# Kernel tuning notes

Measured on AMD Instinct MI355X. Metric: run time of the kernel, lower is better.

Reference implementation:

```python
import jax, jax.numpy as jnp
import numpy as np
from jax import lax

B, N, M, D = 32, 256, 256, 512
NEG = -1e9  # matches deepblast's -1e10-style padding of V borders


def _nw_score(theta, A):
    """Soft (softmax-operator) Needleman-Wunsch terminal score V[N, M].

    theta, A: [N, M]. Recurrence (deepblast _forward_pass):
      V[i, j] = theta[i-1, j-1] + logsumexp(A[i-1, j-1] + V[i-1, j],
                                            V[i-1, j-1],
                                            A[i-1, j-1] + V[i, j-1])
    with V[0, 0] = 0 and borders -inf. Implemented as a row scan with an
    inner column scan (left dependency is sequential within a row).
    """
    n, m = theta.shape
    dt = theta.dtype

    def row_step(prev_row, xs):
        # prev_row: V[i-1, 0..M]  (length m+1)
        th_row, a_row = xs  # each [m]

        def col_step(v_left, c):
            v_diag, v_up, th, a = c
            v = th + jax.nn.logsumexp(jnp.stack([a + v_up, v_diag, a + v_left]))
            return v, v

        _, row = lax.scan(col_step, jnp.asarray(NEG, dt),
                          (prev_row[:-1], prev_row[1:], th_row, a_row))
        new_row = jnp.concatenate([jnp.full((1,), NEG, dt), row])
        return new_row, None

    init = jnp.concatenate([jnp.zeros((1,), dt), jnp.full((m,), NEG, dt)])
    last_row, _ = lax.scan(row_step, init, (theta, A))
    return last_row[-1]  # V[N, M]


def _nw_decode(theta, A):
    # deepblast's decode returns E = dV_t/dtheta (expected alignment matrix);
    # with the softmax operator this is exactly the gradient of the terminal
    # score, so autodiff reproduces the hand-written backward pass.
    return jax.grad(_nw_score, argnums=0)(theta, A)


def setup_inputs() -> dict:
    key = jax.random.key(0)
    k1, k2, k3, k4 = jax.random.split(key, 4)
    s = D ** -0.25  # so bid,bjd dot products are ~N(0, 1)
    zx = jax.random.normal(k1, (B, N, D), jnp.float32) * s
    zy = jax.random.normal(k2, (B, M, D), jnp.float32) * s
    gx = jax.random.normal(k3, (B, N, D), jnp.float32) * s
    gy = jax.random.normal(k4, (B, M, D), jnp.float32) * s
    return {"zx": zx, "zy": zy, "gx": gx, "gy": gy}


def reference(zx, zy, gx, gy):
    theta = jax.nn.softplus(jnp.einsum('bid,bjd->bij', zx, zy))  # [B,N,M]
    A = jax.nn.log_sigmoid(jnp.einsum('bid,bjd->bij', gx, gy))   # [B,N,M]
    aln = jax.vmap(_nw_decode)(theta, A)                          # [B,N,M]
    return aln, theta, A
```

## Files before the change

kernel.cpp:

```cpp
#include <hip/hip_runtime.h>
#include <hip/hip_bf16.h>
#include <hip/hip_fp16.h>
#include <cstdint>
#include <cstddef>

#define BB 32
#define NN 256
#define MM 256
#define DD 512
#define NEGF (-1e9f)
#define LOG2E 1.4426950408889634f
#define SPLN 82176
#define QPLN 82176
#define EPLN 81920

typedef __fp16 h2 __attribute__((ext_vector_type(2)));
typedef float f32x4_t __attribute__((ext_vector_type(4)));
typedef unsigned int u32x4_t __attribute__((ext_vector_type(4)));
typedef short s16x8 __attribute__((ext_vector_type(8)));

__device__ __forceinline__ uint32_t pack_q(float a, float b) {
  h2 r = __builtin_amdgcn_cvt_pkrtz(a, b);
  return __builtin_bit_cast(uint32_t, r);
}
__device__ __forceinline__ float2 unpack_q(uint32_t u) {
  h2 r = __builtin_bit_cast(h2, u);
  return make_float2((float)r.x, (float)r.y);
}
__device__ __forceinline__ float softplus_f(float x) {
  return fmaxf(x, 0.f) + __logf(1.f + __expf(-fabsf(x)));
}
__device__ __forceinline__ float logsig_f(float x) {
  return fminf(x, 0.f) - __logf(1.f + __expf(-fabsf(x)));
}
__device__ __forceinline__ short f2bf(float f) {
  uint32_t u = __builtin_bit_cast(uint32_t, f);
  u += 0x7FFFu + ((u >> 16) & 1u);
  return (short)(u >> 16);
}

#define WAITV(N) do { \
  asm volatile("s_waitcnt vmcnt(" #N ")" ::: "memory"); \
  __builtin_amdgcn_sched_barrier(0); \
} while (0)

#define DRAIN() do { \
  asm volatile("s_waitcnt vmcnt(0) lgkmcnt(0)" ::: "memory"); \
  __builtin_amdgcn_sched_barrier(0); \
} while (0)

#define SBAR() __builtin_amdgcn_sched_barrier(0)

__global__ __launch_bounds__(256) void gemm_mfma(const float* __restrict__ ZX,
                                                 const float* __restrict__ ZY,
                                                 const float* __restrict__ GX,
                                                 const float* __restrict__ GY,
                                                 float* __restrict__ theta,
                                                 float* __restrict__ Amat,
                                                 float* __restrict__ thS,
                                                 float* __restrict__ aS) {
  const int z  = blockIdx.z;
  const int b  = z & 31;
  const int op = z >> 5;
  const int ty = blockIdx.y;
  const int tx = blockIdx.x;
  const float* Xb = (op ? GX : ZX) + (size_t)b * NN * DD;
  const float* Yb = (op ? GY : ZY) + (size_t)b * MM * DD;
  float* outb = (op ? Amat : theta) + (size_t)b * NN * MM;
  float* skb  = (op ? aS : thS) + (size_t)b * SPLN;

  __shared__ short xs[64][40];
  __shared__ short ys[64][40];

  const int tid = threadIdx.x;
  const int l   = tid & 63;
  const int w   = tid >> 6;
  const int r0  = (w >> 1) * 32;
  const int c0  = (w & 1) * 32;
  const int srow = tid >> 2;
  const int scg  = (tid & 3) * 8;

  f32x4_t acc[2][2];
  #pragma unroll
  for (int i = 0; i < 2; ++i)
    #pragma unroll
    for (int j = 0; j < 2; ++j) acc[i][j] = f32x4_t{0.f, 0.f, 0.f, 0.f};

  const int lr = l & 15;
  const int kof = (l >> 4) * 8;

  for (int ks = 0; ks < 16; ++ks) {
    const int k0 = ks * 32;
    const float4 xv0 = *(const float4*)(Xb + (size_t)(ty * 64 + srow) * DD + k0 + scg);
    const float4 xv1 = *(const float4*)(Xb + (size_t)(ty * 64 + srow) * DD + k0 + scg + 4);
    const float4 yv0 = *(const float4*)(Yb + (size_t)(tx * 64 + srow) * DD + k0 + scg);
    const float4 yv1 = *(const float4*)(Yb + (size_t)(tx * 64 + srow) * DD + k0 + scg + 4);
    __syncthreads();
    s16x8 xp, yp;
    xp[0] = f2bf(xv0.x); xp[1] = f2bf(xv0.y); xp[2] = f2bf(xv0.z); xp[3] = f2bf(xv0.w);
    xp[4] = f2bf(xv1.x); xp[5] = f2bf(xv1.y); xp[6] = f2bf(xv1.z); xp[7] = f2bf(xv1.w);
    yp[0] = f2bf(yv0.x); yp[1] = f2bf(yv0.y); yp[2] = f2bf(yv0.z); yp[3] = f2bf(yv0.w);
    yp[4] = f2bf(yv1.x); yp[5] = f2bf(yv1.y); yp[6] = f2bf(yv1.z); yp[7] = f2bf(yv1.w);
    *(s16x8*)&xs[srow][scg] = xp;
    *(s16x8*)&ys[srow][scg] = yp;
    __syncthreads();
    const s16x8 a0 = *(const s16x8*)&xs[r0 + lr][kof];
    const s16x8 a1 = *(const s16x8*)&xs[r0 + 16 + lr][kof];
    const s16x8 b0 = *(const s16x8*)&ys[c0 + lr][kof];
    const s16x8 b1 = *(const s16x8*)&ys[c0 + 16 + lr][kof];
    acc[0][0] = __builtin_amdgcn_mfma_f32_16x16x32_bf16(a0, b0, acc[0][0], 0, 0, 0);
    acc[0][1] = __builtin_amdgcn_mfma_f32_16x16x32_bf16(a0, b1, acc[0][1], 0, 0, 0);
    acc[1][0] = __builtin_amdgcn_mfma_f32_16x16x32_bf16(a1, b0, acc[1][0], 0, 0, 0);
    acc[1][1] = __builtin_amdgcn_mfma_f32_16x16x32_bf16(a1, b1, acc[1][1], 0, 0, 0);
  }

  #pragma unroll
  for (int i = 0; i < 2; ++i) {
    #pragma unroll
    for (int j = 0; j < 2; ++j) {
      #pragma unroll
      for (int r = 0; r < 4; ++r) {
        const int R = ty * 64 + r0 + i * 16 + (l >> 4) * 4 + r;
        const int C = tx * 64 + c0 + j * 16 + (l & 15);
        const float v = acc[i][j][r];
        const float act = (op == 0) ? softplus_f(v) : logsig_f(v);
        outb[(size_t)R * MM + C] = act;
        skb[(size_t)(C + 1 + (R >> 2)) * 256 + R] = act * LOG2E;
      }
    }
  }
}

__global__ __launch_bounds__(64, 1) void nw_wave(const float* __restrict__ thSA,
                                                 const float* __restrict__ aSA,
                                                 u32x4_t* __restrict__ qSA,
                                                 float* __restrict__ eSA) {
  const int b = blockIdx.x;
  const int t = threadIdx.x;
  const float* thS = thSA + (size_t)b * SPLN;
  const float* aS  = aSA  + (size_t)b * SPLN;
  u32x4_t* qS = qSA + (size_t)b * (QPLN / 4);
  float* eSb = eSA + (size_t)b * EPLN;

  __shared__ f32x4_t stg[24][64];

  float vp[4];
  #pragma unroll
  for (int k = 0; k < 4; ++k) vp[k] = NEGF;
  float vu_sh = NEGF, vd_sh = NEGF;

  auto fstage = [&](int rbase, int mlo) {
    #pragma unroll
    for (int q = 0; q < 4; ++q) {
      int m = mlo + q; m = m < 1 ? 1 : (m > 320 ? 320 : m);
      __builtin_amdgcn_global_load_lds((const void*)(thS + (size_t)m * 256 + 4 * t),
                                       (void*)&stg[rbase + q][0], 16, 0, 0);
      __builtin_amdgcn_global_load_lds((const void*)(aS + (size_t)m * 256 + 4 * t),
                                       (void*)&stg[rbase + 4 + q][0], 16, 0, 0);
    }
  };

  fstage(0, 1); fstage(8, 5); fstage(16, 9);
  u32x4_t* qpt = qS + 64 + t;
  for (int h = 0; h < 80; ++h) {
    const int m0 = 1 + 4 * h;
    const int R = (h % 3) * 8;
    if (h == 0)      WAITV(16);
    else if (h == 1) WAITV(20);
    else             WAITV(24);
    f32x4_t thc = stg[R][t], ac = stg[R + 4][t];
    f32x4_t thn, an;
    #pragma unroll
    for (int u = 0; u < 4; ++u) {
      if (u < 3) { thn = stg[R + u + 1][t]; an = stg[R + 4 + u + 1][t]; }
      SBAR();
      const int m = m0 + u;
      const int j = m - t;
      const bool actv = (j >= 1) && (j <= 256);
      float vu_in = vu_sh, vd_in = vd_sh;
      if (t == 0) { vu_in = NEGF; vd_in = (m == 1) ? 0.f : NEGF; }
      float x2v[4], m12[4];
      #pragma unroll
      for (int k = 0; k < 4; ++k) {
        x2v[k] = ac[k] + vp[k];
        const float vdk = (k == 0) ? vd_in : vp[k - 1];
        m12[k] = fmaxf(vdk, x2v[k]);
      }
      float vn[4];
      uint32_t pk[4];
      #pragma unroll
      for (int k = 0; k < 4; ++k) {
        const float vu  = (k == 0) ? vu_in : vn[k - 1];
        const float vdk = (k == 0) ? vd_in : vp[k - 1];
        const float x0 = ac[k] + vu;
        const float mx = fmaxf(x0, m12[k]);
        const float e0 = __builtin_amdgcn_exp2f(x0 - mx);
        const float e1 = __builtin_amdgcn_exp2f(vdk - mx);
        const float e2 = __builtin_amdgcn_exp2f(x2v[k] - mx);
        const float Z  = e0 + e1 + e2;
        const float rz = __builtin_amdgcn_rcpf(Z);
        const float v  = thc[k] + mx + __builtin_amdgcn_logf(Z);
        vn[k] = actv ? v : vp[k];
        pk[k] = pack_q(e0 * rz, e2 * rz);
      }
      qpt[0] = u32x4_t{pk[0], pk[1], pk[2], pk[3]};
      qpt += 64;
      const float nsh = __shfl_up(vn[3], 1);
      vd_sh = vu_sh; vu_sh = nsh;
      #pragma unroll
      for (int k = 0; k < 4; ++k) vp[k] = vn[k];
      if (u < 3) { thc = thn; ac = an; }
    }
    fstage(R, m0 + 12);
  }

  DRAIN();

  float ep[4] = {0.f, 0.f, 0.f, 0.f};
  float sh_e1 = 0.f, sh_e2 = 0.f;
  uint32_t sh_q1 = 0u, sh_q2 = 0u;
  u32x4_t qm1 = u32x4_t{0u, 0u, 0u, 0u};
  const u32x4_t QONE = u32x4_t{0x3C00u, 0x3C00u, 0x3C00u, 0x3C00u};

  auto bstage = [&](int rbase, int Phi) {
    #pragma unroll
    for (int u = 0; u < 4; ++u) {
      int P = Phi - u; P = P < 0 ? 0 : (P > 320 ? 320 : P);
      __builtin_amdgcn_global_load_lds((const void*)(qS + (size_t)P * 64 + t),
                                       (void*)&stg[rbase + u][0], 16, 0, 0);
    }
  };

  bstage(0, 319); bstage(4, 315); bstage(8, 311);
  float* eptr = eSb + 4 * t;
  for (int n = 0; n < 80; ++n) {
    const int R = (n % 3) * 4;
    if (n == 0)      WAITV(8);
    else if (n == 1) WAITV(12);
    else             WAITV(16);
    u32x4_t cur = __builtin_bit_cast(u32x4_t, stg[R][t]);
    u32x4_t nxt;
    #pragma unroll
    for (int u = 0; u < 4; ++u) {
      if (u < 3) nxt = __builtin_bit_cast(u32x4_t, stg[R + u + 1][t]);
      SBAR();
      const int mp = 4 * n + u;
      const int P  = 319 - mp;
      const int j  = P - t;
      const bool actv = (j >= 1) && (j <= 256);
      const bool jok  = (j <= 255);
      const u32x4_t qmm = jok ? qm1 : QONE;
      const uint32_t sq1 = (t == 63) ? 0u : sh_q1;
      const uint32_t sq2 = (t == 63 || !jok) ? 0x3C00u : sh_q2;
      float en[4];
      #pragma unroll
      for (int kk = 0; kk < 4; ++kk) {
        const int k = 3 - kk;
        const uint32_t uA = (k < 3) ? cur[k + 1] : sq1;
        const uint32_t uB = (k < 3) ? qmm[k + 1] : sq2;
        const uint32_t uC = qmm[k];
        const float2 fA = unpack_q(uA);
        const float2 fB = unpack_q(uB);
        const float2 fC = unpack_q(uC);
        const float q1u = fA.x;
        const float q2d = 1.f - fB.x - fB.y;
        const float q3l = fC.y;
        const float eu = (k < 3) ? en[k + 1] : sh_e1;
        const float ed = (k < 3) ? ep[k + 1] : sh_e2;
        const float el = ep[k];
        float E = q1u * eu + q2d * ed + q3l * el;
        if (n == 0 && u == 0 && k == 3) E = (t == 63) ? 1.f : E;
        en[k] = actv ? E : 0.f;
      }
      *(f32x4_t*)eptr = f32x4_t{en[0], en[1], en[2], en[3]};
      eptr += 256;
      const float ne = __shfl_down(en[0], 1);
      sh_e2 = sh_e1; sh_e1 = ne;
      const uint32_t nq = (uint32_t)__shfl_down((int)cur[0], 1);
      sh_q2 = sh_q1; sh_q1 = nq;
      ep[0] = en[0]; ep[1] = en[1]; ep[2] = en[2]; ep[3] = en[3];
      qm1 = cur;
      if (u < 3) cur = nxt;
    }
    bstage(R, 307 - 4 * n);
  }
}

__global__ __launch_bounds__(256) void untwist(const float* __restrict__ eS,
                                               float* __restrict__ aln) {
  const int b  = blockIdx.z;
  const int r0 = blockIdx.y * 64;
  const int c0 = blockIdx.x * 64;
  const int tid = threadIdx.x;
  const float* ep = eS + (size_t)b * EPLN;

  __shared__ float ld[80][65];

  const int lx = tid & 63;
  const int wy = tid >> 6;
  const int mbase = 240 - c0 - (r0 >> 2);
  #pragma unroll
  for (int k = 0; k < 20; ++k) {
    const int p = wy + 4 * k;
    ld[p][lx] = ep[(size_t)(mbase + p) * 256 + r0 + lx];
  }
  __syncthreads();
  #pragma unroll
  for (int k = 0; k < 16; ++k) {
    const int rr = wy + 4 * k;
    aln[(size_t)b * NN * MM + (size_t)(r0 + rr) * MM + c0 + lx] =
        ld[78 - lx - (rr >> 2)][rr];
  }
}

extern "C" void kernel_launch(void* const* d_in, const int* in_sizes, int n_in,
                              void* d_out, int out_size, void* d_ws, size_t ws_size,
                              hipStream_t stream) {
  const float* zx = (const float*)d_in[0];
  const float* zy = (const float*)d_in[1];
  const float* gx = (const float*)d_in[2];
  const float* gy = (const float*)d_in[3];

  float* out   = (float*)d_out;
  float* aln   = out;
  float* theta = out + (size_t)BB * NN * MM;
  float* Amat  = out + (size_t)2 * BB * NN * MM;

  float* ws  = (float*)d_ws;
  float* thS = ws;
  float* aS  = ws + (size_t)BB * SPLN;
  u32x4_t* qS = (u32x4_t*)(ws + (size_t)2 * BB * SPLN);
  float* eS = ws + (size_t)3 * BB * SPLN;

  gemm_mfma<<<dim3(4, 4, 64), 256, 0, stream>>>(zx, zy, gx, gy,
                                                theta, Amat, thS, aS);
  nw_wave<<<BB, 64, 0, stream>>>(thS, aS, qS, eS);
  untwist<<<dim3(4, 4, BB), 256, 0, stream>>>(eS, aln);
}
```

Before: 170.3 us.

## Write backward pass results directly to aln and drop untwist kernel; deepen forward staging

The backward wavefront now scatters each thread's four E values straight into the final aln matrix, using a dummy per-thread slot for inactive lanes. This removes the intermediate skewed E buffer and the separate untwist transpose kernel and its launch. The forward pass stages 8 anti-diagonals per batch instead of 4, doubling the LDS staging area, and the shuffle is moved ahead of the probability packing to overlap its latency. The direct stores are strided by row (non-coalesced), and the backward wait counts were changed to account for the new store traffic.

```diff
diff --git a/kernel.cpp b/kernel.cpp
--- a/kernel.cpp
+++ b/kernel.cpp
@@ -12,7 +12,6 @@
 #define LOG2E 1.4426950408889634f
 #define SPLN 82176
 #define QPLN 82176
-#define EPLN 81920
 
 typedef __fp16 h2 __attribute__((ext_vector_type(2)));
 typedef float f32x4_t __attribute__((ext_vector_type(4)));
@@ -134,45 +133,47 @@
 __global__ __launch_bounds__(64, 1) void nw_wave(const float* __restrict__ thSA,
                                                  const float* __restrict__ aSA,
                                                  u32x4_t* __restrict__ qSA,
-                                                 float* __restrict__ eSA) {
+                                                 float* __restrict__ aln,
+                                                 float* __restrict__ dmpA) {
   const int b = blockIdx.x;
   const int t = threadIdx.x;
   const float* thS = thSA + (size_t)b * SPLN;
   const float* aS  = aSA  + (size_t)b * SPLN;
   u32x4_t* qS = qSA + (size_t)b * (QPLN / 4);
-  float* eSb = eSA + (size_t)b * EPLN;
-
-  __shared__ f32x4_t stg[24][64];
+  float* ALN = aln + (size_t)b * NN * MM;
+  float* dmp = dmpA + (size_t)b * 64 + t;
+
+  __shared__ f32x4_t stg[48][64];
 
   float vp[4];
   #pragma unroll
   for (int k = 0; k < 4; ++k) vp[k] = NEGF;
   float vu_sh = NEGF, vd_sh = NEGF;
 
-  auto fstage = [&](int rbase, int mlo) {
-    #pragma unroll
-    for (int q = 0; q < 4; ++q) {
+  auto fstage8 = [&](int rbase, int mlo) {
+    #pragma unroll
+    for (int q = 0; q < 8; ++q) {
       int m = mlo + q; m = m < 1 ? 1 : (m > 320 ? 320 : m);
       __builtin_amdgcn_global_load_lds((const void*)(thS + (size_t)m * 256 + 4 * t),
                                        (void*)&stg[rbase + q][0], 16, 0, 0);
       __builtin_amdgcn_global_load_lds((const void*)(aS + (size_t)m * 256 + 4 * t),
-                                       (void*)&stg[rbase + 4 + q][0], 16, 0, 0);
+                                       (void*)&stg[rbase + 8 + q][0], 16, 0, 0);
     }
   };
 
-  fstage(0, 1); fstage(8, 5); fstage(16, 9);
+  fstage8(0, 1); fstage8(16, 9); fstage8(32, 17);
   u32x4_t* qpt = qS + 64 + t;
-  for (int h = 0; h < 80; ++h) {
-    const int m0 = 1 + 4 * h;
-    const int R = (h % 3) * 8;
-    if (h == 0)      WAITV(16);
-    else if (h == 1) WAITV(20);
-    else             WAITV(24);
-    f32x4_t thc = stg[R][t], ac = stg[R + 4][t];
+  for (int h = 0; h < 40; ++h) {
+    const int m0 = 1 + 8 * h;
+    const int R = (h % 3) * 16;
+    if (h == 0)      WAITV(32);
+    else if (h == 1) WAITV(40);
+    else             WAITV(48);
+    f32x4_t thc = stg[R][t], ac = stg[R + 8][t];
     f32x4_t thn, an;
     #pragma unroll
-    for (int u = 0; u < 4; ++u) {
-      if (u < 3) { thn = stg[R + u + 1][t]; an = stg[R + 4 + u + 1][t]; }
+    for (int u = 0; u < 8; ++u) {
+      if (u < 7) { thn = stg[R + u + 1][t]; an = stg[R + 8 + u + 1][t]; }
       SBAR();
       const int m = m0 + u;
       const int j = m - t;
@@ -186,8 +187,7 @@
         const float vdk = (k == 0) ? vd_in : vp[k - 1];
         m12[k] = fmaxf(vdk, x2v[k]);
       }
-      float vn[4];
-      uint32_t pk[4];
+      float vn[4], e0v[4], e2v[4], rzv[4];
       #pragma unroll
       for (int k = 0; k < 4; ++k) {
         const float vu  = (k == 0) ? vu_in : vn[k - 1];
@@ -198,20 +198,24 @@
         const float e1 = __builtin_amdgcn_exp2f(vdk - mx);
         const float e2 = __builtin_amdgcn_exp2f(x2v[k] - mx);
         const float Z  = e0 + e1 + e2;
-        const float rz = __builtin_amdgcn_rcpf(Z);
+        rzv[k] = __builtin_amdgcn_rcpf(Z);
         const float v  = thc[k] + mx + __builtin_amdgcn_logf(Z);
         vn[k] = actv ? v : vp[k];
-        pk[k] = pack_q(e0 * rz, e2 * rz);
+        e0v[k] = e0; e2v[k] = e2;
       }
+      const float nsh = __shfl_up(vn[3], 1);
+      uint32_t pk[4];
+      #pragma unroll
+      for (int k = 0; k < 4; ++k)
+        pk[k] = pack_q(e0v[k] * rzv[k], e2v[k] * rzv[k]);
       qpt[0] = u32x4_t{pk[0], pk[1], pk[2], pk[3]};
       qpt += 64;
-      const float nsh = __shfl_up(vn[3], 1);
       vd_sh = vu_sh; vu_sh = nsh;
       #pragma unroll
       for (int k = 0; k < 4; ++k) vp[k] = vn[k];
-      if (u < 3) { thc = thn; ac = an; }
-    }
-    fstage(R, m0 + 12);
+      if (u < 7) { thc = thn; ac = an; }
+    }
+    fstage8(R, m0 + 24);
   }
 
   DRAIN();
@@ -232,12 +236,11 @@
   };
 
   bstage(0, 319); bstage(4, 315); bstage(8, 311);
-  float* eptr = eSb + 4 * t;
   for (int n = 0; n < 80; ++n) {
     const int R = (n % 3) * 4;
     if (n == 0)      WAITV(8);
-    else if (n == 1) WAITV(12);
-    else             WAITV(16);
+    else if (n == 1) WAITV(24);
+    else             WAITV(40);
     u32x4_t cur = __builtin_bit_cast(u32x4_t, stg[R][t]);
     u32x4_t nxt;
     #pragma unroll
@@ -272,44 +275,18 @@
         if (n == 0 && u == 0 && k == 3) E = (t == 63) ? 1.f : E;
         en[k] = actv ? E : 0.f;
       }
-      *(f32x4_t*)eptr = f32x4_t{en[0], en[1], en[2], en[3]};
-      eptr += 256;
       const float ne = __shfl_down(en[0], 1);
+      const uint32_t nq = (uint32_t)__shfl_down((int)cur[0], 1);
+      float* bp = actv ? (ALN + (size_t)(4 * t) * MM + (j - 1)) : dmp;
+      const int st = actv ? MM : 0;
+      bp[0] = en[0]; bp[st] = en[1]; bp[2 * st] = en[2]; bp[3 * st] = en[3];
       sh_e2 = sh_e1; sh_e1 = ne;
-      const uint32_t nq = (uint32_t)__shfl_down((int)cur[0], 1);
       sh_q2 = sh_q1; sh_q1 = nq;
       ep[0] = en[0]; ep[1] = en[1]; ep[2] = en[2]; ep[3] = en[3];
       qm1 = cur;
       if (u < 3) cur = nxt;
     }
     bstage(R, 307 - 4 * n);
-  }
-}
-
-__global__ __launch_bounds__(256) void untwist(const float* __restrict__ eS,
-                                               float* __restrict__ aln) {
-  const int b  = blockIdx.z;
-  const int r0 = blockIdx.y * 64;
-  const int c0 = blockIdx.x * 64;
-  const int tid = threadIdx.x;
-  const float* ep = eS + (size_t)b * EPLN;
-
-  __shared__ float ld[80][65];
-
-  const int lx = tid & 63;
-  const int wy = tid >> 6;
-  const int mbase = 240 - c0 - (r0 >> 2);
-  #pragma unroll
-  for (int k = 0; k < 20; ++k) {
-    const int p = wy + 4 * k;
-    ld[p][lx] = ep[(size_t)(mbase + p) * 256 + r0 + lx];
-  }
-  __syncthreads();
-  #pragma unroll
-  for (int k = 0; k < 16; ++k) {
-    const int rr = wy + 4 * k;
-    aln[(size_t)b * NN * MM + (size_t)(r0 + rr) * MM + c0 + lx] =
-        ld[78 - lx - (rr >> 2)][rr];
   }
 }
 
@@ -330,10 +307,9 @@
   float* thS = ws;
   float* aS  = ws + (size_t)BB * SPLN;
   u32x4_t* qS = (u32x4_t*)(ws + (size_t)2 * BB * SPLN);
-  float* eS = ws + (size_t)3 * BB * SPLN;
+  float* dmp = ws + (size_t)3 * BB * SPLN;
 
   gemm_mfma<<<dim3(4, 4, 64), 256, 0, stream>>>(zx, zy, gx, gy,
                                                 theta, Amat, thS, aS);
-  nw_wave<<<BB, 64, 0, stream>>>(thS, aS, qS, eS);
-  untwist<<<dim3(4, 4, BB), 256, 0, stream>>>(eS, aln);
-}
+  nw_wave<<<BB, 64, 0, stream>>>(thS, aS, qS, aln, dmp);
+}
```

Measured after the change: 173.6 us. No clear change (+1.9%).

## Split NW wavefront across two waves with 2 rows per lane and interleaved skew layout

Applied to the files above, without the earlier changes.

The soft-NW forward and backward wavefronts now run on 128 threads (two waves) per batch instead of one, with each lane owning 2 rows instead of 4. This shortens the serial dependency chain per anti-diagonal step. The two waves exchange boundary values through shared memory with a workgroup barrier every step. Theta and A are interleaved into one skewed plane so a single async load fetches both, and q is stored per-step instead of staged. The cost is more diagonal steps (383 instead of 319), a barrier per step, and larger workspace and untwist footprints.

```diff
diff --git a/kernel.cpp b/kernel.cpp
--- a/kernel.cpp
+++ b/kernel.cpp
@@ -10,9 +10,9 @@
 #define DD 512
 #define NEGF (-1e9f)
 #define LOG2E 1.4426950408889634f
-#define SPLN 82176
-#define QPLN 82176
-#define EPLN 81920
+#define SKWN 196608
+#define QPN  98304
+#define EPN  98304
 
 typedef __fp16 h2 __attribute__((ext_vector_type(2)));
 typedef float f32x4_t __attribute__((ext_vector_type(4)));
@@ -49,7 +49,12 @@
   __builtin_amdgcn_sched_barrier(0); \
 } while (0)
 
-#define SBAR() __builtin_amdgcn_sched_barrier(0)
+#define STEPBAR() do { \
+  asm volatile("s_waitcnt lgkmcnt(0)" ::: "memory"); \
+  __builtin_amdgcn_sched_barrier(0); \
+  __builtin_amdgcn_s_barrier(); \
+  asm volatile("" ::: "memory"); \
+} while (0)
 
 __global__ __launch_bounds__(256) void gemm_mfma(const float* __restrict__ ZX,
                                                  const float* __restrict__ ZY,
@@ -57,8 +62,7 @@
                                                  const float* __restrict__ GY,
                                                  float* __restrict__ theta,
                                                  float* __restrict__ Amat,
-                                                 float* __restrict__ thS,
-                                                 float* __restrict__ aS) {
+                                                 float* __restrict__ skw) {
   const int z  = blockIdx.z;
   const int b  = z & 31;
   const int op = z >> 5;
@@ -67,7 +71,7 @@
   const float* Xb = (op ? GX : ZX) + (size_t)b * NN * DD;
   const float* Yb = (op ? GY : ZY) + (size_t)b * MM * DD;
   float* outb = (op ? Amat : theta) + (size_t)b * NN * MM;
-  float* skb  = (op ? aS : thS) + (size_t)b * SPLN;
+  float* skb  = skw + (size_t)b * SKWN;
 
   __shared__ short xs[64][40];
   __shared__ short ys[64][40];
@@ -125,164 +129,176 @@
         const float v = acc[i][j][r];
         const float act = (op == 0) ? softplus_f(v) : logsig_f(v);
         outb[(size_t)R * MM + C] = act;
-        skb[(size_t)(C + 1 + (R >> 2)) * 256 + R] = act * LOG2E;
+        const int m = (C + 1) + (R >> 1);
+        skb[(size_t)m * 512 + ((R >> 1) << 2) + (op ? 2 : 0) + (R & 1)] =
+            act * LOG2E;
       }
     }
   }
 }
 
-__global__ __launch_bounds__(64, 1) void nw_wave(const float* __restrict__ thSA,
-                                                 const float* __restrict__ aSA,
-                                                 u32x4_t* __restrict__ qSA,
-                                                 float* __restrict__ eSA) {
+__global__ __launch_bounds__(128, 1) void nw_wave(const float* __restrict__ skwA,
+                                                  uint32_t* __restrict__ qSA,
+                                                  float* __restrict__ eSA) {
   const int b = blockIdx.x;
   const int t = threadIdx.x;
-  const float* thS = thSA + (size_t)b * SPLN;
-  const float* aS  = aSA  + (size_t)b * SPLN;
-  u32x4_t* qS = qSA + (size_t)b * (QPLN / 4);
-  float* eSb = eSA + (size_t)b * EPLN;
-
-  __shared__ f32x4_t stg[24][64];
-
-  float vp[4];
-  #pragma unroll
-  for (int k = 0; k < 4; ++k) vp[k] = NEGF;
+  const int w64 = (t >> 6) << 6;
+  const float* skw = skwA + (size_t)b * SKWN;
+  uint32_t* qS = qSA + (size_t)b * QPN;
+  float* eSb = eSA + (size_t)b * EPN;
+
+  __shared__ f32x4_t stg[12][128];
+  __shared__ uint32_t qstg[12][256];
+  __shared__ float xv[3];
+  __shared__ float xe[3];
+  __shared__ uint32_t xq[3];
+
+  if (t < 3) { xv[t] = NEGF; xe[t] = 0.f; xq[t] = 0u; }
+  __syncthreads();
+
+  float vp[2] = {NEGF, NEGF};
   float vu_sh = NEGF, vd_sh = NEGF;
 
   auto fstage = [&](int rbase, int mlo) {
     #pragma unroll
     for (int q = 0; q < 4; ++q) {
-      int m = mlo + q; m = m < 1 ? 1 : (m > 320 ? 320 : m);
-      __builtin_amdgcn_global_load_lds((const void*)(thS + (size_t)m * 256 + 4 * t),
-                                       (void*)&stg[rbase + q][0], 16, 0, 0);
-      __builtin_amdgcn_global_load_lds((const void*)(aS + (size_t)m * 256 + 4 * t),
-                                       (void*)&stg[rbase + 4 + q][0], 16, 0, 0);
+      int m = mlo + q; m = m < 1 ? 1 : (m > 383 ? 383 : m);
+      __builtin_amdgcn_global_load_lds((const void*)(skw + (size_t)m * 512 + 4 * t),
+                                       (void*)&stg[rbase + q][w64], 16, 0, 0);
     }
   };
 
-  fstage(0, 1); fstage(8, 5); fstage(16, 9);
-  u32x4_t* qpt = qS + 64 + t;
-  for (int h = 0; h < 80; ++h) {
+  fstage(0, 1); fstage(4, 5); fstage(8, 9);
+  for (int h = 0; h < 96; ++h) {
     const int m0 = 1 + 4 * h;
-    const int R = (h % 3) * 8;
-    if (h == 0)      WAITV(16);
-    else if (h == 1) WAITV(20);
-    else             WAITV(24);
-    f32x4_t thc = stg[R][t], ac = stg[R + 4][t];
-    f32x4_t thn, an;
+    const int R = (h % 3) * 4;
+    if (h == 0)      WAITV(8);
+    else if (h == 1) WAITV(12);
+    else             WAITV(16);
+    f32x4_t c4 = stg[R][t];
+    f32x4_t n4;
     #pragma unroll
     for (int u = 0; u < 4; ++u) {
-      if (u < 3) { thn = stg[R + u + 1][t]; an = stg[R + 4 + u + 1][t]; }
-      SBAR();
+      if (u < 3) n4 = stg[R + u + 1][t];
       const int m = m0 + u;
+      const float xvr1 = xv[(m + 2) % 3];
+      const float xvr2 = xv[(m + 1) % 3];
+      __builtin_amdgcn_sched_barrier(0);
       const int j = m - t;
       const bool actv = (j >= 1) && (j <= 256);
-      float vu_in = vu_sh, vd_in = vd_sh;
+      float vu_in = (t == 64) ? xvr1 : vu_sh;
+      float vd_in = (t == 64) ? xvr2 : vd_sh;
       if (t == 0) { vu_in = NEGF; vd_in = (m == 1) ? 0.f : NEGF; }
-      float x2v[4], m12[4];
+      float vn[2];
+      uint32_t pk[2];
       #pragma unroll
-      for (int k = 0; k < 4; ++k) {
-        x2v[k] = ac[k] + vp[k];
-        const float vdk = (k == 0) ? vd_in : vp[k - 1];
-        m12[k] = fmaxf(vdk, x2v[k]);
-      }
-      float vn[4];
-      uint32_t pk[4];
-      #pragma unroll
-      for (int k = 0; k < 4; ++k) {
-        const float vu  = (k == 0) ? vu_in : vn[k - 1];
-        const float vdk = (k == 0) ? vd_in : vp[k - 1];
-        const float x0 = ac[k] + vu;
-        const float mx = fmaxf(x0, m12[k]);
+      for (int k = 0; k < 2; ++k) {
+        const float vu  = (k == 0) ? vu_in : vn[0];
+        const float vdk = (k == 0) ? vd_in : vp[0];
+        const float vl  = vp[k];
+        const float a  = c4[2 + k];
+        const float th = c4[k];
+        const float x0 = a + vu;
+        const float x2 = a + vl;
+        const float mx = fmaxf(fmaxf(x0, vdk), x2);
         const float e0 = __builtin_amdgcn_exp2f(x0 - mx);
         const float e1 = __builtin_amdgcn_exp2f(vdk - mx);
-        const float e2 = __builtin_amdgcn_exp2f(x2v[k] - mx);
+        const float e2 = __builtin_amdgcn_exp2f(x2 - mx);
         const float Z  = e0 + e1 + e2;
         const float rz = __builtin_amdgcn_rcpf(Z);
-        const float v  = thc[k] + mx + __builtin_amdgcn_logf(Z);
+        const float v  = th + mx + __builtin_amdgcn_logf(Z);
         vn[k] = actv ? v : vp[k];
         pk[k] = pack_q(e0 * rz, e2 * rz);
       }
-      qpt[0] = u32x4_t{pk[0], pk[1], pk[2], pk[3]};
-      qpt += 64;
-      const float nsh = __shfl_up(vn[3], 1);
+      const float nsh = __shfl_up(vn[1], 1);
+      const int ms = (m <= 383) ? m : 0;
+      *(uint2*)(qS + (size_t)ms * 256 + 2 * t) = make_uint2(pk[0], pk[1]);
+      if (t == 63) xv[m % 3] = vn[1];
       vd_sh = vu_sh; vu_sh = nsh;
-      #pragma unroll
-      for (int k = 0; k < 4; ++k) vp[k] = vn[k];
-      if (u < 3) { thc = thn; ac = an; }
+      vp[0] = vn[0]; vp[1] = vn[1];
+      if (u < 3) c4 = n4;
+      STEPBAR();
     }
     fstage(R, m0 + 12);
   }
 
   DRAIN();
-
-  float ep[4] = {0.f, 0.f, 0.f, 0.f};
+  __builtin_amdgcn_s_barrier();
+
+  float ep[2] = {0.f, 0.f};
   float sh_e1 = 0.f, sh_e2 = 0.f;
   uint32_t sh_q1 = 0u, sh_q2 = 0u;
-  u32x4_t qm1 = u32x4_t{0u, 0u, 0u, 0u};
-  const u32x4_t QONE = u32x4_t{0x3C00u, 0x3C00u, 0x3C00u, 0x3C00u};
-
-  auto bstage = [&](int rbase, int Phi) {
+  uint32_t qm1[2] = {0u, 0u};
+
+  auto qstage = [&](int rbase, int Phi) {
+    #pragma unroll
+    for (int q = 0; q < 4; ++q) {
+      int P = Phi - q; P = P < 0 ? 0 : (P > 383 ? 383 : P);
+      const uint32_t* s0 = qS + (size_t)P * 256 + ((t >> 6) << 7) + (t & 63);
+      __builtin_amdgcn_global_load_lds((const void*)s0,
+                                       (void*)&qstg[rbase + q][(t >> 6) << 7], 4, 0, 0);
+      __builtin_amdgcn_global_load_lds((const void*)(s0 + 64),
+                                       (void*)&qstg[rbase + q][((t >> 6) << 7) + 64], 4, 0, 0);
+    }
+  };
+
+  qstage(0, 383); qstage(4, 379); qstage(8, 375);
+  for (int n = 0; n < 96; ++n) {
+    const int R = (n % 3) * 4;
+    if (n == 0)      WAITV(16);
+    else if (n == 1) WAITV(20);
+    else             WAITV(24);
+    uint2 cur = *(uint2*)&qstg[R][2 * t];
+    uint2 nxt;
     #pragma unroll
     for (int u = 0; u < 4; ++u) {
-      int P = Phi - u; P = P < 0 ? 0 : (P > 320 ? 320 : P);
-      __builtin_amdgcn_global_load_lds((const void*)(qS + (size_t)P * 64 + t),
-                                       (void*)&stg[rbase + u][0], 16, 0, 0);
-    }
-  };
-
-  bstage(0, 319); bstage(4, 315); bstage(8, 311);
-  float* eptr = eSb + 4 * t;
-  for (int n = 0; n < 80; ++n) {
-    const int R = (n % 3) * 4;
-    if (n == 0)      WAITV(8);
-    else if (n == 1) WAITV(12);
-    else             WAITV(16);
-    u32x4_t cur = __builtin_bit_cast(u32x4_t, stg[R][t]);
-    u32x4_t nxt;
-    #pragma unroll
-    for (int u = 0; u < 4; ++u) {
-      if (u < 3) nxt = __builtin_bit_cast(u32x4_t, stg[R + u + 1][t]);
-      SBAR();
+      if (u < 3) nxt = *(uint2*)&qstg[R + u + 1][2 * t];
       const int mp = 4 * n + u;
-      const int P  = 319 - mp;
-      const int j  = P - t;
+      const int P  = 383 - mp;
+      const float    xer1 = xe[(mp + 2) % 3];
+      const float    xer2 = xe[(mp + 1) % 3];
+      const uint32_t xqr1 = xq[(mp + 2) % 3];
+      const uint32_t xqr2 = xq[(mp + 1) % 3];
+      __builtin_amdgcn_sched_barrier(0);
+      const int j = P - t;
       const bool actv = (j >= 1) && (j <= 256);
       const bool jok  = (j <= 255);
-      const u32x4_t qmm = jok ? qm1 : QONE;
-      const uint32_t sq1 = (t == 63) ? 0u : sh_q1;
-      const uint32_t sq2 = (t == 63 || !jok) ? 0x3C00u : sh_q2;
-      float en[4];
-      #pragma unroll
-      for (int kk = 0; kk < 4; ++kk) {
-        const int k = 3 - kk;
-        const uint32_t uA = (k < 3) ? cur[k + 1] : sq1;
-        const uint32_t uB = (k < 3) ? qmm[k + 1] : sq2;
-        const uint32_t uC = qmm[k];
-        const float2 fA = unpack_q(uA);
-        const float2 fB = unpack_q(uB);
-        const float2 fC = unpack_q(uC);
-        const float q1u = fA.x;
-        const float q2d = 1.f - fB.x - fB.y;
-        const float q3l = fC.y;
-        const float eu = (k < 3) ? en[k + 1] : sh_e1;
-        const float ed = (k < 3) ? ep[k + 1] : sh_e2;
-        const float el = ep[k];
-        float E = q1u * eu + q2d * ed + q3l * el;
-        if (n == 0 && u == 0 && k == 3) E = (t == 63) ? 1.f : E;
-        en[k] = actv ? E : 0.f;
+      const float se1 = (t == 63) ? xer1 : sh_e1;
+      const float se2 = (t == 63) ? xer2 : sh_e2;
+      uint32_t sq1 = (t == 63) ? xqr1 : sh_q1;
+      uint32_t sq2 = (t == 63) ? xqr2 : sh_q2;
+      sq1 = (t == 127) ? 0u : sq1;
+      sq2 = (t == 127 || !jok) ? 0x3C00u : sq2;
+      const uint32_t qm0v = jok ? qm1[0] : 0x3C00u;
+      const uint32_t qm1v = jok ? qm1[1] : 0x3C00u;
+      float en[2];
+      {
+        const float2 fA = unpack_q(sq1);
+        const float2 fB = unpack_q(sq2);
+        const float2 fC = unpack_q(qm1v);
+        float E = fA.x * se1 + (1.f - fB.x - fB.y) * se2 + fC.y * ep[1];
+        if (n == 0 && u == 0) E = (t == 127) ? 1.f : E;
+        en[1] = actv ? E : 0.f;
       }
-      *(f32x4_t*)eptr = f32x4_t{en[0], en[1], en[2], en[3]};
-      eptr += 256;
+      {
+        const float2 fA = unpack_q(cur.y);
+        const float2 fB = unpack_q(qm1v);
+        const float2 fC = unpack_q(qm0v);
+        const float E = fA.x * en[1] + (1.f - fB.x - fB.y) * ep[1] + fC.y * ep[0];
+        en[0] = actv ? E : 0.f;
+      }
       const float ne = __shfl_down(en[0], 1);
+      const uint32_t nq = (uint32_t)__shfl_down((int)cur.x, 1);
+      *(float2*)(eSb + (size_t)mp * 256 + 2 * t) = make_float2(en[0], en[1]);
+      if (t == 64) { xe[mp % 3] = en[0]; xq[mp % 3] = cur.x; }
       sh_e2 = sh_e1; sh_e1 = ne;
-      const uint32_t nq = (uint32_t)__shfl_down((int)cur[0], 1);
       sh_q2 = sh_q1; sh_q1 = nq;
-      ep[0] = en[0]; ep[1] = en[1]; ep[2] = en[2]; ep[3] = en[3];
-      qm1 = cur;
+      ep[0] = en[0]; ep[1] = en[1];
+      qm1[0] = cur.x; qm1[1] = cur.y;
       if (u < 3) cur = nxt;
-    }
-    bstage(R, 307 - 4 * n);
+      STEPBAR();
+    }
+    qstage(R, 371 - 4 * n);
   }
 }
 
@@ -292,24 +308,24 @@
   const int r0 = blockIdx.y * 64;
   const int c0 = blockIdx.x * 64;
   const int tid = threadIdx.x;
-  const float* ep = eS + (size_t)b * EPLN;
-
-  __shared__ float ld[80][65];
+  const float* ep = eS + (size_t)b * EPN;
+
+  __shared__ float ld[95][65];
 
   const int lx = tid & 63;
   const int wy = tid >> 6;
-  const int mbase = 240 - c0 - (r0 >> 2);
+  const int mbase = 288 - c0 - (r0 >> 1);
   #pragma unroll
-  for (int k = 0; k < 20; ++k) {
+  for (int k = 0; k < 24; ++k) {
     const int p = wy + 4 * k;
-    ld[p][lx] = ep[(size_t)(mbase + p) * 256 + r0 + lx];
+    if (p < 95) ld[p][lx] = ep[(size_t)(mbase + p) * 256 + r0 + lx];
   }
   __syncthreads();
   #pragma unroll
   for (int k = 0; k < 16; ++k) {
     const int rr = wy + 4 * k;
     aln[(size_t)b * NN * MM + (size_t)(r0 + rr) * MM + c0 + lx] =
-        ld[78 - lx - (rr >> 2)][rr];
+        ld[94 - lx - (rr >> 1)][rr];
   }
 }
 
@@ -327,13 +343,12 @@
   float* Amat  = out + (size_t)2 * BB * NN * MM;
 
   float* ws  = (float*)d_ws;
-  float* thS = ws;
-  float* aS  = ws + (size_t)BB * SPLN;
-  u32x4_t* qS = (u32x4_t*)(ws + (size_t)2 * BB * SPLN);
-  float* eS = ws + (size_t)3 * BB * SPLN;
+  float* skw = ws;
+  uint32_t* qS = (uint32_t*)(ws + (size_t)BB * SKWN);
+  float* eS = ws + (size_t)BB * SKWN + (size_t)BB * QPN;
 
   gemm_mfma<<<dim3(4, 4, 64), 256, 0, stream>>>(zx, zy, gx, gy,
-                                                theta, Amat, thS, aS);
-  nw_wave<<<BB, 64, 0, stream>>>(thS, aS, qS, eS);
+                                                theta, Amat, skw);
+  nw_wave<<<BB, 128, 0, stream>>>(skw, qS, eS);
   untwist<<<dim3(4, 4, BB), 256, 0, stream>>>(eS, aln);
 }
```

Measured after the change: 273.3 us. 60.5% more time.

## Specialize wavefront DP loops into boundary and full-interior segments, vectorize skew store

Applied to the files above, without the earlier changes.

Splits the forward and backward anti-diagonal wavefront loops into edge and interior segments via a compile-time flag. The interior segments drop the per-cell active-range checks and selects. The forward step now issues the cross-lane shuffle before packing probabilities, so the serial dependency chain is shorter, and the GEMM epilogue writes the skewed plane with one float4 store instead of four scalar stores. This assumes wavefronts 16..63 are fully interior for all 64 lanes, which holds for this skew geometry, and the cost is larger code size.

```diff
diff --git a/kernel.cpp b/kernel.cpp
--- a/kernel.cpp
+++ b/kernel.cpp
@@ -3,6 +3,7 @@
 #include <hip/hip_fp16.h>
 #include <cstdint>
 #include <cstddef>
+#include <type_traits>
 
 #define BB 32
 #define NN 256
@@ -118,15 +119,21 @@
   for (int i = 0; i < 2; ++i) {
     #pragma unroll
     for (int j = 0; j < 2; ++j) {
+      const int Rb = ty * 64 + r0 + i * 16 + (l >> 4) * 4;
+      const int C  = tx * 64 + c0 + j * 16 + (l & 15);
+      float4 av;
       #pragma unroll
       for (int r = 0; r < 4; ++r) {
-        const int R = ty * 64 + r0 + i * 16 + (l >> 4) * 4 + r;
-        const int C = tx * 64 + c0 + j * 16 + (l & 15);
         const float v = acc[i][j][r];
-        const float act = (op == 0) ? softplus_f(v) : logsig_f(v);
-        outb[(size_t)R * MM + C] = act;
-        skb[(size_t)(C + 1 + (R >> 2)) * 256 + R] = act * LOG2E;
-      }
+        ((float*)&av)[r] = (op == 0) ? softplus_f(v) : logsig_f(v);
+      }
+      #pragma unroll
+      for (int r = 0; r < 4; ++r)
+        outb[(size_t)(Rb + r) * MM + C] = ((float*)&av)[r];
+      float4 sv;
+      #pragma unroll
+      for (int r = 0; r < 4; ++r) ((float*)&sv)[r] = ((float*)&av)[r] * LOG2E;
+      *(float4*)&skb[(size_t)(C + 1 + (Rb >> 2)) * 256 + Rb] = sv;
     }
   }
 }
@@ -162,7 +169,9 @@
 
   fstage(0, 1); fstage(8, 5); fstage(16, 9);
   u32x4_t* qpt = qS + 64 + t;
-  for (int h = 0; h < 80; ++h) {
+
+  auto fwd_seg = [&](const int h, const auto fullc) {
+    constexpr bool FULL = decltype(fullc)::value;
     const int m0 = 1 + 4 * h;
     const int R = (h % 3) * 8;
     if (h == 0)      WAITV(16);
@@ -175,44 +184,48 @@
       if (u < 3) { thn = stg[R + u + 1][t]; an = stg[R + 4 + u + 1][t]; }
       SBAR();
       const int m = m0 + u;
-      const int j = m - t;
-      const bool actv = (j >= 1) && (j <= 256);
       float vu_in = vu_sh, vd_in = vd_sh;
       if (t == 0) { vu_in = NEGF; vd_in = (m == 1) ? 0.f : NEGF; }
-      float x2v[4], m12[4];
-      #pragma unroll
-      for (int k = 0; k < 4; ++k) {
-        x2v[k] = ac[k] + vp[k];
-        const float vdk = (k == 0) ? vd_in : vp[k - 1];
-        m12[k] = fmaxf(vdk, x2v[k]);
-      }
-      float vn[4];
-      uint32_t pk[4];
+      bool actv = true;
+      if constexpr (!FULL) {
+        const int j = m - t;
+        actv = (j >= 1) && (j <= 256);
+      }
+      float vn[4], e0v[4], e2v[4], rzv[4];
       #pragma unroll
       for (int k = 0; k < 4; ++k) {
         const float vu  = (k == 0) ? vu_in : vn[k - 1];
         const float vdk = (k == 0) ? vd_in : vp[k - 1];
         const float x0 = ac[k] + vu;
-        const float mx = fmaxf(x0, m12[k]);
+        const float x2 = ac[k] + vp[k];
+        const float mx = fmaxf(fmaxf(x0, vdk), x2);
         const float e0 = __builtin_amdgcn_exp2f(x0 - mx);
         const float e1 = __builtin_amdgcn_exp2f(vdk - mx);
-        const float e2 = __builtin_amdgcn_exp2f(x2v[k] - mx);
+        const float e2 = __builtin_amdgcn_exp2f(x2 - mx);
         const float Z  = e0 + e1 + e2;
-        const float rz = __builtin_amdgcn_rcpf(Z);
+        rzv[k] = __builtin_amdgcn_rcpf(Z);
         const float v  = thc[k] + mx + __builtin_amdgcn_logf(Z);
-        vn[k] = actv ? v : vp[k];
-        pk[k] = pack_q(e0 * rz, e2 * rz);
-      }
+        vn[k] = FULL ? v : (actv ? v : vp[k]);
+        e0v[k] = e0; e2v[k] = e2;
+      }
+      const float nsh = __shfl_up(vn[3], 1);
+      uint32_t pk[4];
+      #pragma unroll
+      for (int k = 0; k < 4; ++k)
+        pk[k] = pack_q(e0v[k] * rzv[k], e2v[k] * rzv[k]);
       qpt[0] = u32x4_t{pk[0], pk[1], pk[2], pk[3]};
       qpt += 64;
-      const float nsh = __shfl_up(vn[3], 1);
       vd_sh = vu_sh; vu_sh = nsh;
       #pragma unroll
       for (int k = 0; k < 4; ++k) vp[k] = vn[k];
       if (u < 3) { thc = thn; ac = an; }
     }
     fstage(R, m0 + 12);
-  }
+  };
+
+  for (int h = 0; h < 16; ++h)  fwd_seg(h, std::integral_constant<bool, false>{});
+  for (int h = 16; h < 64; ++h) fwd_seg(h, std::integral_constant<bool, true>{});
+  for (int h = 64; h < 80; ++h) fwd_seg(h, std::integral_constant<bool, false>{});
 
   DRAIN();
 
@@ -232,8 +245,9 @@
   };
 
   bstage(0, 319); bstage(4, 315); bstage(8, 311);
-  float* eptr = eSb + 4 * t;
-  for (int n = 0; n < 80; ++n) {
+
+  auto bwd_seg = [&](const int n, const auto fullc) {
+    constexpr bool FULL = decltype(fullc)::value;
     const int R = (n % 3) * 4;
     if (n == 0)      WAITV(8);
     else if (n == 1) WAITV(12);
@@ -246,10 +260,13 @@
       SBAR();
       const int mp = 4 * n + u;
       const int P  = 319 - mp;
-      const int j  = P - t;
-      const bool actv = (j >= 1) && (j <= 256);
-      const bool jok  = (j <= 255);
-      const u32x4_t qmm = jok ? qm1 : QONE;
+      bool actv = true, jok = true;
+      if constexpr (!FULL) {
+        const int j = P - t;
+        actv = (j >= 1) && (j <= 256);
+        jok  = (j <= 255);
+      }
+      const u32x4_t qmm = FULL ? qm1 : (jok ? qm1 : QONE);
       const uint32_t sq1 = (t == 63) ? 0u : sh_q1;
       const uint32_t sq2 = (t == 63 || !jok) ? 0x3C00u : sh_q2;
       float en[4];
@@ -269,21 +286,26 @@
         const float ed = (k < 3) ? ep[k + 1] : sh_e2;
         const float el = ep[k];
         float E = q1u * eu + q2d * ed + q3l * el;
-        if (n == 0 && u == 0 && k == 3) E = (t == 63) ? 1.f : E;
-        en[k] = actv ? E : 0.f;
-      }
-      *(f32x4_t*)eptr = f32x4_t{en[0], en[1], en[2], en[3]};
-      eptr += 256;
+        if constexpr (!FULL) {
+          if (n == 0 && u == 0 && k == 3) E = (t == 63) ? 1.f : E;
+        }
+        en[k] = FULL ? E : (actv ? E : 0.f);
+      }
       const float ne = __shfl_down(en[0], 1);
+      const uint32_t nq = (uint32_t)__shfl_down((int)cur[0], 1);
+      *(f32x4_t*)(eSb + (size_t)mp * 256 + 4 * t) = f32x4_t{en[0], en[1], en[2], en[3]};
       sh_e2 = sh_e1; sh_e1 = ne;
-      const uint32_t nq = (uint32_t)__shfl_down((int)cur[0], 1);
       sh_q2 = sh_q1; sh_q1 = nq;
       ep[0] = en[0]; ep[1] = en[1]; ep[2] = en[2]; ep[3] = en[3];
       qm1 = cur;
       if (u < 3) cur = nxt;
     }
     bstage(R, 307 - 4 * n);
-  }
+  };
+
+  for (int n = 0; n < 16; ++n)  bwd_seg(n, std::integral_constant<bool, false>{});
+  for (int n = 16; n < 64; ++n) bwd_seg(n, std::integral_constant<bool, true>{});
+  for (int n = 64; n < 80; ++n) bwd_seg(n, std::integral_constant<bool, false>{});
 }
 
 __global__ __launch_bounds__(256) void untwist(const float* __restrict__ eS,
```

After: 161.3 us. -5.3%, faster.
